# Kernel optimization log

Hardware: AMD Instinct MI355X
Metric: run time of the kernel (lower is better)

The kernel has to match this reference:

```python
import jax, jax.numpy as jnp
import numpy as np

T = 1.0        # temperature (init kwarg t)
NEG = -1e9     # finite mask value: exp(NEG - max) underflows to exactly 0 in fp32


def setup_inputs() -> dict:
    key = jax.random.key(0)
    k1, k2 = jax.random.split(key)
    B, L, D = 48, 17, 256
    x = jax.random.normal(k1, (B, L, D), dtype=jnp.float32)
    label = jax.random.randint(k2, (B,), 0, 8, dtype=jnp.int64)
    return {"input": x, "label": label}


def _loss(x, label):
    B, L, D = x.shape
    M = B * (L - 1)
    # F.normalize(dim=2)
    xn = x / jnp.maximum(jnp.linalg.norm(x, axis=2, keepdims=True), 1e-12)
    anchors = xn[:, 0]                         # [B, D]
    toks = xn[:, 1:].reshape(M, D)             # [M, D], row r belongs to sample owner[r]
    owner = jnp.repeat(jnp.arange(B), L - 1)   # [M]
    same = label[:, None] == label[owner][None, :]   # [B, M] same-class mask per anchor
    neg = ~same                                      # negative-column mask per anchor

    s_anc = (anchors @ toks.T) / T   # [B, M] anchor-vs-token scores
    s_tok = (toks @ toks.T) / T      # [M, M] token-vs-token scores

    # anchor_consistent_score_unify: softmax of s_anc over negative columns only
    a_logits = jnp.where(neg, s_anc, NEG)                       # [B, M]
    log_denom = jax.scipy.special.logsumexp(a_logits, axis=1)   # [B]  log sum_c exp(s_anc)
    a_unify = jnp.exp(a_logits - log_denom[:, None])            # [B, M], 0 at masked cols
    # positive_consistent_score_unify: exp(s_tok) / anchor denom (NOT a row softmax)
    p_unify = jnp.exp(s_tok[None, :, :] - log_denom[:, None, None])  # [B, M, M]

    # second-level Softmax / LogSoftmax applied to the unify VALUES, neg cols only
    a_m = jnp.where(neg, a_unify, NEG)                 # [B, M]
    p_m = jnp.where(neg[:, None, :], p_unify, NEG)     # [B, M, M]
    log_a = jax.nn.log_softmax(a_m, axis=1)            # [B, M]
    log_p = jax.nn.log_softmax(p_m, axis=2)            # [B, M, M]
    sm_a = jnp.exp(log_a)
    sm_p = jnp.exp(log_p)

    col = neg[:, None, :]
    # KL(input=log_a repeated over rows, target=sm_p), elementwise t*(log t - inp)
    kl1 = jnp.where(col, sm_p * (log_p - log_a[:, None, :]), 0.0).sum(axis=2)          # [B, M]
    # KL(input=log_p, target=sm_a repeated over rows)
    kl2 = jnp.where(col, sm_a[:, None, :] * (log_a[:, None, :] - log_p), 0.0).sum(axis=2)

    row = same.astype(x.dtype)              # positive rows for anchor i
    P = row.sum(axis=1)                     # batchmean divisor = #positive rows
    l1 = (kl1 * row).sum(axis=1) / P
    l2 = (kl2 * row).sum(axis=1) / P
    return jnp.mean(0.5 * l1 + 0.5 * l2)


def reference(input, label):
    return _loss(input, label)
```

## Files before the change

kernel.cpp:

```cpp
#include <hip/hip_runtime.h>
#include <math.h>

#define Bn 48
#define Ln 17
#define Dn 256
#define Mn 768
#define NS 2
#define LDA 76

static __device__ __forceinline__ double pexp(double e) {
  return 1.0 + e*(1.0 + e*(0.5 + e*((1.0/6.0) + e*((1.0/24.0) + e*(1.0/120.0)))));
}

static __device__ __forceinline__ double blockReduce16(double v, double* red) {
  __syncthreads();
  #pragma unroll
  for (int o = 32; o > 0; o >>= 1) v += __shfl_down(v, o, 64);
  int lane = threadIdx.x & 63, wid = threadIdx.x >> 6;
  if (lane == 0) red[wid] = v;
  __syncthreads();
  double r = 0.0;
  #pragma unroll
  for (int w = 0; w < 16; ++w) r += red[w];
  return r;
}

static __device__ __forceinline__ int src_row_m(int m) {
  if (m < Bn) return m * Ln;
  int t = m - Bn;
  return (t >> 4) * Ln + (t & 15) + 1;
}
static __device__ __forceinline__ int src_row_n(int n) {
  return (n >> 4) * Ln + (n & 15) + 1;
}

__global__ __launch_bounds__(256) void kA_gemm(const float* __restrict__ x,
                                               float* __restrict__ EA,
                                               float* __restrict__ E,
                                               float* __restrict__ out) {
  __shared__ float As[16][LDA];
  __shared__ float Bs[16][LDA];
  __shared__ float nA[64], nB[64];
  int tid = threadIdx.x;
  if (blockIdx.x == 0 && blockIdx.y == 0 && tid == 0) out[0] = 0.f;
  int m0 = blockIdx.y * 64, n0 = blockIdx.x * 64;
  int r  = tid >> 2, cq = tid & 3;
  int mrow = m0 + r;
  int gm = (mrow < 816) ? src_row_m(mrow) : 0;
  int gn = src_row_n(n0 + r);
  const float* pa = x + gm * Dn + cq * 4;
  const float* pb = x + gn * Dn + cq * 4;
  float4 ra = *(const float4*)pa;
  float4 rb = *(const float4*)pb;
  float ssa = 0.f, ssb = 0.f;
  float c[4][4];
  #pragma unroll
  for (int i = 0; i < 4; ++i)
    #pragma unroll
    for (int j = 0; j < 4; ++j) c[i][j] = 0.f;
  int tx = tid & 15, ty = tid >> 4;

  for (int t = 0; t < 16; ++t) {
    __syncthreads();
    int kb = cq * 4;
    As[kb+0][r] = ra.x; As[kb+1][r] = ra.y; As[kb+2][r] = ra.z; As[kb+3][r] = ra.w;
    Bs[kb+0][r] = rb.x; Bs[kb+1][r] = rb.y; Bs[kb+2][r] = rb.z; Bs[kb+3][r] = rb.w;
    ssa += ra.x*ra.x + ra.y*ra.y + ra.z*ra.z + ra.w*ra.w;
    ssb += rb.x*rb.x + rb.y*rb.y + rb.z*rb.z + rb.w*rb.w;
    __syncthreads();
    if (t < 15) {
      ra = *(const float4*)(pa + (t + 1) * 16);
      rb = *(const float4*)(pb + (t + 1) * 16);
    }
    #pragma unroll
    for (int k = 0; k < 16; ++k) {
      float4 a4 = *(const float4*)&As[k][ty * 4];
      float4 b4 = *(const float4*)&Bs[k][tx * 4];
      float av[4] = {a4.x, a4.y, a4.z, a4.w};
      float bv[4] = {b4.x, b4.y, b4.z, b4.w};
      #pragma unroll
      for (int i = 0; i < 4; ++i)
        #pragma unroll
        for (int j = 0; j < 4; ++j) c[i][j] = fmaf(av[i], bv[j], c[i][j]);
    }
  }
  ssa += __shfl_xor(ssa, 1, 64); ssa += __shfl_xor(ssa, 2, 64);
  ssb += __shfl_xor(ssb, 1, 64); ssb += __shfl_xor(ssb, 2, 64);
  if (cq == 0) { nA[r] = ssa; nB[r] = ssb; }
  __syncthreads();
  double ia[4], ib[4];
  #pragma unroll
  for (int i = 0; i < 4; ++i) ia[i] = 1.0 / sqrt((double)nA[ty * 4 + i]);
  #pragma unroll
  for (int j = 0; j < 4; ++j) ib[j] = 1.0 / sqrt((double)nB[tx * 4 + j]);
  #pragma unroll
  for (int i = 0; i < 4; ++i) {
    int m = m0 + ty * 4 + i;
    if (m < 816) {
      #pragma unroll
      for (int j = 0; j < 4; ++j) {
        int n = n0 + tx * 4 + j;
        float s = (float)((double)c[i][j] * ia[i] * ib[j]);
        float ev = __expf(s);
        if (m < Bn) EA[m * Mn + n] = ev;
        else        E[(m - Bn) * Mn + n] = ev;
      }
    }
  }
}

__global__ __launch_bounds__(1024, 2) void kB_i(const float* __restrict__ EA,
                                                const float* __restrict__ E,
                                                const int* __restrict__ label,
                                                float* __restrict__ out) {
  __shared__ double2 sp[Mn];
  __shared__ double red[16];
  __shared__ int lab[Bn];
  int slice = blockIdx.x, i = blockIdx.y;
  int tid = threadIdx.x;
  int lane = tid & 63, w = tid >> 6;
  if (tid < Bn) lab[tid] = label[tid];
  __syncthreads();
  int li = lab[i];

  bool has = (tid < Mn);
  bool neg = has && (lab[tid >> 4] != li);
  double eav = has ? (double)EA[i * Mn + tid] : 0.0;
  double s1 = blockReduce16(neg ? eav : 0.0, red);
  double ci = 1.0 / s1;
  double a = ci * eav;
  double p = pexp(a);
  if (has) { sp[tid].x = neg ? a : 0.0; sp[tid].y = neg ? p : 0.0; }
  double t2a = blockReduce16(neg ? p : 0.0, red);
  double t2b = blockReduce16(neg ? p * a : 0.0, red);
  double inv_s2 = 1.0 / t2a;
  double Evi = t2b * inv_s2;
  unsigned long long nm = __ballot(lane < Bn && lab[lane] != li);
  int cnt = 64 - __popcll(nm | 0xFFFF000000000000ull);

  int kb0 = lane >> 4;
  double tsum = 0.0;
  for (int bj = slice; bj < Bn; bj += NS) {
    if (lab[bj] != li) continue;
    const float* Ej = E + (bj * 16 + w) * Mn + lane;
    float Evv[12];
    #pragma unroll
    for (int it = 0; it < 12; ++it) Evv[it] = Ej[64 * it];
    double A = 0.0, Bv = 0.0, C = 0.0, D2 = 0.0;
    #pragma unroll
    for (int it = 0; it < 12; ++it) {
      double m = (double)((nm >> (kb0 + 4 * it)) & 1ull);
      double e = ci * (double)Evv[it];
      double wx = pexp(e);
      double wm = wx * m;
      double2 s = sp[lane + 64 * it];
      A  = fma(wm, e, A);
      Bv = fma(wx, s.x, Bv);
      C += wm;
      D2 = fma(s.y, e, D2);
    }
    #pragma unroll
    for (int o = 32; o > 0; o >>= 1) {
      A  += __shfl_xor(A,  o, 64);
      Bv += __shfl_xor(Bv, o, 64);
      C  += __shfl_xor(C,  o, 64);
      D2 += __shfl_xor(D2, o, 64);
    }
    tsum += (A - Bv) / C - D2 * inv_s2 + Evi;
  }

  __syncthreads();
  if (lane == 0) red[w] = tsum;
  __syncthreads();
  if (tid == 0) {
    double s = 0.0;
    #pragma unroll
    for (int ww = 0; ww < 16; ++ww) s += red[ww];
    atomicAdd(out, (float)(s / (1536.0 * (double)cnt)));
  }
}

extern "C" void kernel_launch(void* const* d_in, const int* in_sizes, int n_in,
                              void* d_out, int out_size, void* d_ws, size_t ws_size,
                              hipStream_t stream) {
  const float* x   = (const float*)d_in[0];
  const int* label = (const int*)d_in[1];
  float* out = (float*)d_out;

  char* ws = (char*)d_ws;
  size_t off = 0;
  auto alloc = [&](size_t bytes) -> void* {
    void* p = ws + off;
    off = (off + bytes + 255) & ~(size_t)255;
    return p;
  };
  float* EA = (float*)alloc((size_t)Bn * Mn * sizeof(float));
  float* E  = (float*)alloc((size_t)Mn * Mn * sizeof(float));

  kA_gemm<<<dim3(12, 13), 256, 0, stream>>>(x, EA, E, out);
  kB_i<<<dim3(NS, Bn), 1024, 0, stream>>>(EA, E, label, out);
}
```

Baseline: 89.55 us.

## Use split-bf16 MFMA for the Gram GEMM instead of FP32 FMA tiles

The first kernel now loads each 64-row tile's full K=256 slab into shared memory once, splits every fp32 value into bf16 hi and lo parts, and computes the dot products with three bf16 MFMA 16x16x32 instructions per step (hi*hi, hi*lo, lo*hi). This replaces the scalar FP32 FMA outer-product loop and its 16 synchronised K-steps. The goal is to move the GEMM onto matrix cores while keeping near-fp32 accuracy. The cost is roughly 135KB of LDS per block, which limits occupancy, plus extra conversion work.

```diff
diff --git a/kernel.cpp b/kernel.cpp
--- a/kernel.cpp
+++ b/kernel.cpp
@@ -6,7 +6,20 @@
 #define Dn 256
 #define Mn 768
 #define NS 2
-#define LDA 76
+#define LDK 264
+
+typedef __attribute__((ext_vector_type(8))) short frag8;
+typedef __attribute__((ext_vector_type(4))) float fragc;
+typedef __attribute__((ext_vector_type(4))) short short4v;
+
+static __device__ __forceinline__ short f2bf(float f) {
+  unsigned u = __float_as_uint(f);
+  unsigned r = (u + 0x7FFFu + ((u >> 16) & 1u)) >> 16;
+  return (short)r;
+}
+static __device__ __forceinline__ float bf2f(short h) {
+  return __uint_as_float(((unsigned)(unsigned short)h) << 16);
+}
 
 static __device__ __forceinline__ double pexp(double e) {
   return 1.0 + e*(1.0 + e*(0.5 + e*((1.0/6.0) + e*((1.0/24.0) + e*(1.0/120.0)))));
@@ -38,69 +51,85 @@
                                                float* __restrict__ EA,
                                                float* __restrict__ E,
                                                float* __restrict__ out) {
-  __shared__ float As[16][LDA];
-  __shared__ float Bs[16][LDA];
+  __shared__ short Ahi[64 * LDK];
+  __shared__ short Alo[64 * LDK];
+  __shared__ short Bhi[64 * LDK];
+  __shared__ short Blo[64 * LDK];
   __shared__ float nA[64], nB[64];
   int tid = threadIdx.x;
   if (blockIdx.x == 0 && blockIdx.y == 0 && tid == 0) out[0] = 0.f;
   int m0 = blockIdx.y * 64, n0 = blockIdx.x * 64;
-  int r  = tid >> 2, cq = tid & 3;
-  int mrow = m0 + r;
-  int gm = (mrow < 816) ? src_row_m(mrow) : 0;
-  int gn = src_row_n(n0 + r);
-  const float* pa = x + gm * Dn + cq * 4;
-  const float* pb = x + gn * Dn + cq * 4;
-  float4 ra = *(const float4*)pa;
-  float4 rb = *(const float4*)pb;
-  float ssa = 0.f, ssb = 0.f;
-  float c[4][4];
-  #pragma unroll
-  for (int i = 0; i < 4; ++i)
-    #pragma unroll
-    for (int j = 0; j < 4; ++j) c[i][j] = 0.f;
-  int tx = tid & 15, ty = tid >> 4;
-
-  for (int t = 0; t < 16; ++t) {
-    __syncthreads();
-    int kb = cq * 4;
-    As[kb+0][r] = ra.x; As[kb+1][r] = ra.y; As[kb+2][r] = ra.z; As[kb+3][r] = ra.w;
-    Bs[kb+0][r] = rb.x; Bs[kb+1][r] = rb.y; Bs[kb+2][r] = rb.z; Bs[kb+3][r] = rb.w;
-    ssa += ra.x*ra.x + ra.y*ra.y + ra.z*ra.z + ra.w*ra.w;
-    ssb += rb.x*rb.x + rb.y*rb.y + rb.z*rb.z + rb.w*rb.w;
-    __syncthreads();
-    if (t < 15) {
-      ra = *(const float4*)(pa + (t + 1) * 16);
-      rb = *(const float4*)(pb + (t + 1) * 16);
-    }
-    #pragma unroll
-    for (int k = 0; k < 16; ++k) {
-      float4 a4 = *(const float4*)&As[k][ty * 4];
-      float4 b4 = *(const float4*)&Bs[k][tx * 4];
-      float av[4] = {a4.x, a4.y, a4.z, a4.w};
-      float bv[4] = {b4.x, b4.y, b4.z, b4.w};
-      #pragma unroll
-      for (int i = 0; i < 4; ++i)
-        #pragma unroll
-        for (int j = 0; j < 4; ++j) c[i][j] = fmaf(av[i], bv[j], c[i][j]);
-    }
-  }
-  ssa += __shfl_xor(ssa, 1, 64); ssa += __shfl_xor(ssa, 2, 64);
-  ssb += __shfl_xor(ssb, 1, 64); ssb += __shfl_xor(ssb, 2, 64);
-  if (cq == 0) { nA[r] = ssa; nB[r] = ssb; }
-  __syncthreads();
+
+  {
+    int r = tid >> 2, cq = tid & 3;
+    int mrow = m0 + r;
+    int gm = (mrow < 816) ? src_row_m(mrow) : 0;
+    int gn = src_row_n(n0 + r);
+    const float4* pa = (const float4*)(x + gm * Dn) + cq * 16;
+    const float4* pb = (const float4*)(x + gn * Dn) + cq * 16;
+    float ssa = 0.f, ssb = 0.f;
+    #pragma unroll
+    for (int c4 = 0; c4 < 16; ++c4) {
+      float4 fa = pa[c4];
+      float4 fb = pb[c4];
+      ssa += fa.x*fa.x + fa.y*fa.y + fa.z*fa.z + fa.w*fa.w;
+      ssb += fb.x*fb.x + fb.y*fb.y + fb.z*fb.z + fb.w*fb.w;
+      int col = cq * 64 + c4 * 4;
+      short4v ah, al, bh, bl;
+      ah.x = f2bf(fa.x); al.x = f2bf(fa.x - bf2f(ah.x));
+      ah.y = f2bf(fa.y); al.y = f2bf(fa.y - bf2f(ah.y));
+      ah.z = f2bf(fa.z); al.z = f2bf(fa.z - bf2f(ah.z));
+      ah.w = f2bf(fa.w); al.w = f2bf(fa.w - bf2f(ah.w));
+      bh.x = f2bf(fb.x); bl.x = f2bf(fb.x - bf2f(bh.x));
+      bh.y = f2bf(fb.y); bl.y = f2bf(fb.y - bf2f(bh.y));
+      bh.z = f2bf(fb.z); bl.z = f2bf(fb.z - bf2f(bh.z));
+      bh.w = f2bf(fb.w); bl.w = f2bf(fb.w - bf2f(bh.w));
+      *(short4v*)&Ahi[r * LDK + col] = ah;
+      *(short4v*)&Alo[r * LDK + col] = al;
+      *(short4v*)&Bhi[r * LDK + col] = bh;
+      *(short4v*)&Blo[r * LDK + col] = bl;
+    }
+    ssa += __shfl_xor(ssa, 1, 64); ssa += __shfl_xor(ssa, 2, 64);
+    ssb += __shfl_xor(ssb, 1, 64); ssb += __shfl_xor(ssb, 2, 64);
+    if ((tid & 3) == 0) { nA[r] = ssa; nB[r] = ssb; }
+  }
+  __syncthreads();
+
+  int lane = tid & 63, w = tid >> 6;
+  int ml = lane & 15, q = lane >> 4;
+  fragc acc[4];
+  #pragma unroll
+  for (int s = 0; s < 4; ++s) acc[s] = (fragc){0.f, 0.f, 0.f, 0.f};
+  int arow = (w * 16 + ml) * LDK;
+  #pragma unroll
+  for (int s = 0; s < 8; ++s) {
+    int ko = s * 32 + q * 8;
+    frag8 ah = *(const frag8*)&Ahi[arow + ko];
+    frag8 al = *(const frag8*)&Alo[arow + ko];
+    #pragma unroll
+    for (int sub = 0; sub < 4; ++sub) {
+      int brow = (sub * 16 + ml) * LDK;
+      frag8 bh = *(const frag8*)&Bhi[brow + ko];
+      frag8 bl = *(const frag8*)&Blo[brow + ko];
+      acc[sub] = __builtin_amdgcn_mfma_f32_16x16x32_bf16(ah, bh, acc[sub], 0, 0, 0);
+      acc[sub] = __builtin_amdgcn_mfma_f32_16x16x32_bf16(ah, bl, acc[sub], 0, 0, 0);
+      acc[sub] = __builtin_amdgcn_mfma_f32_16x16x32_bf16(al, bh, acc[sub], 0, 0, 0);
+    }
+  }
+
   double ia[4], ib[4];
   #pragma unroll
-  for (int i = 0; i < 4; ++i) ia[i] = 1.0 / sqrt((double)nA[ty * 4 + i]);
-  #pragma unroll
-  for (int j = 0; j < 4; ++j) ib[j] = 1.0 / sqrt((double)nB[tx * 4 + j]);
-  #pragma unroll
-  for (int i = 0; i < 4; ++i) {
-    int m = m0 + ty * 4 + i;
-    if (m < 816) {
-      #pragma unroll
-      for (int j = 0; j < 4; ++j) {
-        int n = n0 + tx * 4 + j;
-        float s = (float)((double)c[i][j] * ia[i] * ib[j]);
+  for (int rg = 0; rg < 4; ++rg) ia[rg] = 1.0 / sqrt((double)nA[w * 16 + q * 4 + rg]);
+  #pragma unroll
+  for (int sub = 0; sub < 4; ++sub) ib[sub] = 1.0 / sqrt((double)nB[sub * 16 + ml]);
+  #pragma unroll
+  for (int sub = 0; sub < 4; ++sub) {
+    int n = n0 + sub * 16 + ml;
+    #pragma unroll
+    for (int rg = 0; rg < 4; ++rg) {
+      int m = m0 + w * 16 + q * 4 + rg;
+      if (m < 816) {
+        float s = (float)((double)acc[sub][rg] * ia[rg] * ib[sub]);
         float ev = __expf(s);
         if (m < Bn) EA[m * Mn + n] = ev;
         else        E[(m - Bn) * Mn + n] = ev;
```

Result: faster. 83.33 us (-6.9%).
